# Kernel optimization log

Hardware: AMD Instinct MI355X
Metric: run time of the kernel (lower is better)

The kernel has to match this reference:

```python
import jax, jax.numpy as jnp
import numpy as np

N, E, C_IN, C_OUT, NHEADS = 100000, 1600000, 128, 128, 4


def setup_inputs() -> dict:
    key = jax.random.key(0)
    k1, k2, k3, k4 = jax.random.split(key, 4)
    x = jax.random.normal(k1, (N, C_IN), dtype=jnp.float32)
    edge_index = jax.random.randint(k2, (2, E), 0, N, dtype=jnp.int32)
    batch_slices_x = jnp.array([0, N], dtype=jnp.int32)
    # glorot-style init scale
    weight = jax.random.normal(k3, (C_IN, C_OUT), dtype=jnp.float32) * (1.0 / np.sqrt(C_IN))
    att_weight = jax.random.normal(k4, (1, NHEADS, 2 * (C_OUT // NHEADS)), dtype=jnp.float32) * 0.1
    return {"x": x, "edge_index": edge_index, "batch_slices_x": batch_slices_x,
            "weight": weight, "att_weight": att_weight}


def reference(x, edge_index, batch_slices_x, weight, att_weight):
    # Eval-mode VotePoolLayer: hard attention via per-source-node argmax (scatter_max),
    # cat head-combine, no bias, att_act = identity, then graph pruning (relabel=False).
    n = x.shape[0]
    nheads = att_weight.shape[1]
    c1h = att_weight.shape[2] // 2  # out_channels per head

    h = (x @ weight).reshape(n, nheads, c1h)  # (N, H, c)
    w_j = att_weight[0, :, :c1h]              # (H, c) weights for source (x_j)
    w_i = att_weight[0, :, c1h:]              # (H, c) weights for target (x_i)
    # alpha[e,h] = sum_c h[src[e],h,c]*w_j[h,c] + h[dst[e],h,c]*w_i[h,c]
    s_j = jnp.einsum('nhc,hc->nh', h, w_j)    # (N, H)
    s_i = jnp.einsum('nhc,hc->nh', h, w_i)    # (N, H)

    src, dst = edge_index[0], edge_index[1]
    alpha = s_j[src] + s_i[dst]               # (E, H)

    # scatter_max argmax over edges grouped by src, per head -> one-hot alpha
    e = alpha.shape[0]
    seg_max = jax.ops.segment_max(alpha, src, num_segments=n)  # (N, H)
    is_max = alpha == seg_max[src]                             # (E, H)
    eids = jnp.arange(e, dtype=jnp.int32)[:, None]             # (E, 1)
    cand = jnp.where(is_max, eids, jnp.int32(e))
    seg_argmax = jax.ops.segment_min(cand, src, num_segments=n)  # (N, H) edge ids
    alpha_1hot = (eids == seg_argmax[src]).astype(h.dtype)       # (E, H)

    # message passing: weighted source features, scatter-add at destination
    msg = h[src] * alpha_1hot[:, :, None]                        # (E, H, c)
    out = jax.ops.segment_sum(msg, dst, num_segments=n)          # (N, H, c)
    out = out.reshape(n, nheads * c1h)                           # cat combine

    # edge selection (eval branch): alpha.sum(dim=1) > 0
    edge_select = alpha_1hot.sum(axis=1) > 0                     # (E,)

    # prune (relabel=False): nodes = unique(dst[edge_select]); keep edges with both
    # endpoints in node set; zero out features of the selected nodes.
    node_mask = jnp.zeros(n, dtype=jnp.int32).at[dst].max(edge_select.astype(jnp.int32)) > 0
    edge_keep = node_mask[src] & node_mask[dst]                  # (E,) subgraph edge mask
    x_out = jnp.where(node_mask[:, None], jnp.float32(0), out)

    return x_out, edge_keep, node_mask, batch_slices_x
```

## Files before the change

kernel.cpp:

```cpp
#include <hip/hip_runtime.h>
#include <stdint.h>

typedef unsigned long long u64;
typedef unsigned int u32;
typedef unsigned short u16;
typedef u32 u32x4 __attribute__((ext_vector_type(4)));
typedef float f32x4 __attribute__((ext_vector_type(4)));
typedef int i32x4 __attribute__((ext_vector_type(4)));

#define CIN 128
#define NN 100000
#define EE 1600000

__device__ __forceinline__ float bf2f(u16 v) {
    union { u32 u; float f; } cv;
    cv.u = ((u32)v) << 16;
    return cv.f;
}

__device__ __forceinline__ u16 f2bf(float f) {
    u32 b = __float_as_uint(f);
    return (u16)((b + 0x7FFFu + ((b >> 16) & 1u)) >> 16);
}

__device__ __forceinline__ u16 mono16(u16 b) {
    return (b & 0x8000u) ? (u16)~b : (u16)(b | 0x8000u);
}

__global__ __launch_bounds__(256, 4) void k_s(const u16* __restrict__ x,
                                              const u16* __restrict__ W,
                                              const u16* __restrict__ att,
                                              ushort4* __restrict__ sib,
                                              u32x4* __restrict__ seg16, int n_seg16,
                                              int* __restrict__ nm, int n_nodes) {
    int stride = gridDim.x * blockDim.x;
    int tid = blockIdx.x * blockDim.x + threadIdx.x;
    u32x4 z = { 0, 0, 0, 0 };
    for (int i = tid; i < n_seg16; i += stride) __builtin_nontemporal_store(z, &seg16[i]);
    for (int i = tid; i < n_nodes; i += stride) nm[i] = 0;

    __shared__ float Vl[512];
    for (int slot = threadIdx.x; slot < 512; slot += 256) {
        int k = slot >> 2, head = slot & 3;
        float acc = 0.0f;
        #pragma unroll
        for (int c = 0; c < 32; ++c)
            acc += bf2f(W[k * CIN + head * 32 + c]) * bf2f(att[head * 64 + 32 + c]);
        Vl[slot] = acc;
    }
    __syncthreads();

    for (int n = tid; n < n_nodes; n += stride) {
        const uint4* row = (const uint4*)(x + (size_t)n * CIN);
        float acc[4];
        #pragma unroll
        for (int h = 0; h < 4; ++h) acc[h] = 0.0f;
        #pragma unroll 4
        for (int q = 0; q < 16; ++q) {
            uint4 v = row[q];
            u32 w[4] = { v.x, v.y, v.z, v.w };
            #pragma unroll
            for (int j = 0; j < 4; ++j) {
                float x0 = bf2f((u16)(w[j] & 0xFFFFu));
                float x1 = bf2f((u16)(w[j] >> 16));
                int k0 = q * 8 + j * 2;
                #pragma unroll
                for (int h = 0; h < 4; ++h) acc[h] += x0 * Vl[k0 * 4 + h];
                #pragma unroll
                for (int h = 0; h < 4; ++h) acc[h] += x1 * Vl[(k0 + 1) * 4 + h];
            }
        }
        ushort4 a;
        a.x = mono16(f2bf(acc[0])); a.y = mono16(f2bf(acc[1]));
        a.z = mono16(f2bf(acc[2])); a.w = mono16(f2bf(acc[3]));
        sib[n] = a;
    }
}

__global__ __launch_bounds__(256) void k_edge(const int* __restrict__ ei,
                                              const ushort4* __restrict__ sib,
                                              u64* __restrict__ seg,
                                              u32x4* __restrict__ xout16, int n_xout16,
                                              int n_edges) {
    int t = blockIdx.x * blockDim.x + threadIdx.x;
    int stride = gridDim.x * blockDim.x;
    u32x4 z = { 0, 0, 0, 0 };
    for (int i = t; i < n_xout16; i += stride) __builtin_nontemporal_store(z, &xout16[i]);

    int e = t;
    if (e >= n_edges) return;
    int src = __builtin_nontemporal_load(ei + e);
    int dst = __builtin_nontemporal_load(ei + n_edges + e);
    ushort4 m = sib[dst];
    u64 lo = ((u64)(0x1FFFFFu - (u32)e) << 27) | ((u64)(u32)dst << 10);
    u64* r = seg + (size_t)src * 4;
    ulonglong2 c01 = *(const ulonglong2*)(r);
    ulonglong2 c23 = *(const ulonglong2*)(r + 2);
    u64 k0 = ((u64)m.x << 48) | lo;
    u64 k1 = ((u64)m.y << 48) | lo;
    u64 k2 = ((u64)m.z << 48) | lo;
    u64 k3 = ((u64)m.w << 48) | lo;
    if (k0 > c01.x) atomicMax(&r[0], k0);
    if (k1 > c01.y) atomicMax(&r[1], k1);
    if (k2 > c23.x) atomicMax(&r[2], k2);
    if (k3 > c23.y) atomicMax(&r[3], k3);
}

__global__ void k_select(const u64* __restrict__ seg,
                         int* __restrict__ nm, int n4) {
    int t = blockIdx.x * blockDim.x + threadIdx.x;
    if (t >= n4) return;
    u64 m = seg[t];
    if (m) nm[(int)((m >> 10) & 0x1FFFFu)] = 1;
}

__global__ void k_final(const int* __restrict__ ei, const int* __restrict__ nm,
                        const int* __restrict__ slices, float* __restrict__ out,
                        int n_edges, int n_nodes, int ek_off, int nm_off, int sl_off) {
    int t = blockIdx.x * blockDim.x + threadIdx.x;
    int e0 = 4 * t;
    if (e0 < n_edges) {
        i32x4 srcs = __builtin_nontemporal_load(((const i32x4*)ei) + t);
        i32x4 dsts = __builtin_nontemporal_load(((const i32x4*)(ei + n_edges)) + t);
        f32x4 v;
        v.x = (nm[srcs.x] & nm[dsts.x]) ? 1.0f : 0.0f;
        v.y = (nm[srcs.y] & nm[dsts.y]) ? 1.0f : 0.0f;
        v.z = (nm[srcs.z] & nm[dsts.z]) ? 1.0f : 0.0f;
        v.w = (nm[srcs.w] & nm[dsts.w]) ? 1.0f : 0.0f;
        __builtin_nontemporal_store(v, &((f32x4*)(out + ek_off))[t]);
    }
    if (t < n_nodes) out[nm_off + t] = nm[t] ? 1.0f : 0.0f;
    if (t < 2) out[sl_off + t] = (float)slices[t];
}

extern "C" void kernel_launch(void* const* d_in, const int* in_sizes, int n_in,
                              void* d_out, int out_size, void* d_ws, size_t ws_size,
                              hipStream_t stream) {
    const u16* x = nullptr; const int* ei = nullptr; const int* sl = nullptr;
    const u16* W = nullptr; const u16* att = nullptr;
    for (int i = 0; i < n_in; ++i) {
        switch (in_sizes[i]) {
            case NN * CIN:   x   = (const u16*)d_in[i]; break;
            case 2 * EE:     ei  = (const int*)d_in[i]; break;
            case 2:          sl  = (const int*)d_in[i]; break;
            case CIN * CIN:  W   = (const u16*)d_in[i]; break;
            case 256:        att = (const u16*)d_in[i]; break;
            default: break;
        }
    }
    if (!x || !ei || !sl || !W || !att) return;

    float* out = (float*)d_out;
    const int N = NN;
    const int E = EE;
    const int N4 = N * 4;

    const int ek_off = N * CIN;
    const int nm_off = ek_off + E;
    const int sl_off = nm_off + N;

    char* ws = (char*)d_ws;
    ushort4* sib = (ushort4*)(ws);
    int*     nm  = (int*)    (ws + (size_t)N * 8);
    u64*     seg = (u64*)    (ws + (size_t)N * 12);

    const int n_xout16 = N * CIN / 4;
    const int n_seg16  = N4 / 2;

    k_s<<<1280, 256, 0, stream>>>(x, W, att, sib,
                                  (u32x4*)seg, n_seg16, nm, N);
    k_edge<<<(E + 255) / 256, 256, 0, stream>>>(ei, sib, seg,
                                                (u32x4*)out, n_xout16, E);
    k_select<<<(N4 + 255) / 256, 256, 0, stream>>>(seg, nm, N4);
    k_final<<<(E / 4 + 255) / 256, 256, 0, stream>>>(ei, nm, sl, out, E, N, ek_off, nm_off, sl_off);
}
```

Measured before the change: 197.8 us.

## Fuse select and final passes via cooperative grid sync; two edges per thread

Merges the node-select kernel and the final edge-mask kernel into one cooperative kernel. A grid-wide sync separates the phase that marks selected nodes from the phase that writes the edge, node-mask and slice outputs, which removes one kernel launch and its gap. The edge kernel now handles two edges per thread with vectorized index loads, for more memory-level parallelism per thread. The cooperative launch relies on all 1563 blocks being co-resident, and the grid sync adds its own barrier cost.

Result: slower. 389.2 us (+96.7%).

```diff
diff --git a/kernel.cpp b/kernel.cpp
--- a/kernel.cpp
+++ b/kernel.cpp
@@ -1,5 +1,8 @@
 #include <hip/hip_runtime.h>
+#include <hip/hip_cooperative_groups.h>
 #include <stdint.h>
+
+namespace cg = cooperative_groups;
 
 typedef unsigned long long u64;
 typedef unsigned int u32;
@@ -7,6 +10,7 @@
 typedef u32 u32x4 __attribute__((ext_vector_type(4)));
 typedef float f32x4 __attribute__((ext_vector_type(4)));
 typedef int i32x4 __attribute__((ext_vector_type(4)));
+typedef int i32x2 __attribute__((ext_vector_type(2)));
 
 #define CIN 128
 #define NN 100000
@@ -87,39 +91,57 @@
     u32x4 z = { 0, 0, 0, 0 };
     for (int i = t; i < n_xout16; i += stride) __builtin_nontemporal_store(z, &xout16[i]);
 
-    int e = t;
-    if (e >= n_edges) return;
-    int src = __builtin_nontemporal_load(ei + e);
-    int dst = __builtin_nontemporal_load(ei + n_edges + e);
-    ushort4 m = sib[dst];
-    u64 lo = ((u64)(0x1FFFFFu - (u32)e) << 27) | ((u64)(u32)dst << 10);
-    u64* r = seg + (size_t)src * 4;
-    ulonglong2 c01 = *(const ulonglong2*)(r);
-    ulonglong2 c23 = *(const ulonglong2*)(r + 2);
-    u64 k0 = ((u64)m.x << 48) | lo;
-    u64 k1 = ((u64)m.y << 48) | lo;
-    u64 k2 = ((u64)m.z << 48) | lo;
-    u64 k3 = ((u64)m.w << 48) | lo;
-    if (k0 > c01.x) atomicMax(&r[0], k0);
-    if (k1 > c01.y) atomicMax(&r[1], k1);
-    if (k2 > c23.x) atomicMax(&r[2], k2);
-    if (k3 > c23.y) atomicMax(&r[3], k3);
-}
-
-__global__ void k_select(const u64* __restrict__ seg,
-                         int* __restrict__ nm, int n4) {
+    int e0 = 2 * t;
+    if (e0 >= n_edges) return;
+    i32x2 s2 = __builtin_nontemporal_load(((const i32x2*)ei) + t);
+    i32x2 d2 = __builtin_nontemporal_load(((const i32x2*)(ei + n_edges)) + t);
+    ushort4 m0 = sib[d2.x];
+    ushort4 m1 = sib[d2.y];
+    u64* r0 = seg + (size_t)s2.x * 4;
+    u64* r1 = seg + (size_t)s2.y * 4;
+
+    {
+        ulonglong2 c01 = *(const ulonglong2*)(r0);
+        ulonglong2 c23 = *(const ulonglong2*)(r0 + 2);
+        u64 lo = ((u64)(0x1FFFFFu - (u32)e0) << 27) | ((u64)(u32)d2.x << 10);
+        u64 k0 = ((u64)m0.x << 48) | lo;
+        u64 k1 = ((u64)m0.y << 48) | lo;
+        u64 k2 = ((u64)m0.z << 48) | lo;
+        u64 k3 = ((u64)m0.w << 48) | lo;
+        if (k0 > c01.x) atomicMax(&r0[0], k0);
+        if (k1 > c01.y) atomicMax(&r0[1], k1);
+        if (k2 > c23.x) atomicMax(&r0[2], k2);
+        if (k3 > c23.y) atomicMax(&r0[3], k3);
+    }
+    {
+        ulonglong2 c01 = *(const ulonglong2*)(r1);
+        ulonglong2 c23 = *(const ulonglong2*)(r1 + 2);
+        u64 lo = ((u64)(0x1FFFFFu - (u32)(e0 + 1)) << 27) | ((u64)(u32)d2.y << 10);
+        u64 k0 = ((u64)m1.x << 48) | lo;
+        u64 k1 = ((u64)m1.y << 48) | lo;
+        u64 k2 = ((u64)m1.z << 48) | lo;
+        u64 k3 = ((u64)m1.w << 48) | lo;
+        if (k0 > c01.x) atomicMax(&r1[0], k0);
+        if (k1 > c01.y) atomicMax(&r1[1], k1);
+        if (k2 > c23.x) atomicMax(&r1[2], k2);
+        if (k3 > c23.y) atomicMax(&r1[3], k3);
+    }
+}
+
+__global__ __launch_bounds__(256) void k_sf(const int* __restrict__ ei,
+                                            const u64* __restrict__ seg,
+                                            int* nm,
+                                            const int* __restrict__ slices,
+                                            float* __restrict__ out,
+                                            int n4, int n_edges, int n_nodes,
+                                            int ek_off, int nm_off, int sl_off) {
     int t = blockIdx.x * blockDim.x + threadIdx.x;
-    if (t >= n4) return;
-    u64 m = seg[t];
-    if (m) nm[(int)((m >> 10) & 0x1FFFFu)] = 1;
-}
-
-__global__ void k_final(const int* __restrict__ ei, const int* __restrict__ nm,
-                        const int* __restrict__ slices, float* __restrict__ out,
-                        int n_edges, int n_nodes, int ek_off, int nm_off, int sl_off) {
-    int t = blockIdx.x * blockDim.x + threadIdx.x;
-    int e0 = 4 * t;
-    if (e0 < n_edges) {
+    if (t < n4) {
+        u64 m = seg[t];
+        if (m) nm[(int)((m >> 10) & 0x1FFFFu)] = 1;
+    }
+    cg::this_grid().sync();
+    if (4 * t < n_edges) {
         i32x4 srcs = __builtin_nontemporal_load(((const i32x4*)ei) + t);
         i32x4 dsts = __builtin_nontemporal_load(((const i32x4*)(ei + n_edges)) + t);
         f32x4 v;
@@ -153,11 +175,11 @@
     float* out = (float*)d_out;
     const int N = NN;
     const int E = EE;
-    const int N4 = N * 4;
-
-    const int ek_off = N * CIN;
-    const int nm_off = ek_off + E;
-    const int sl_off = nm_off + N;
+    int N4 = N * 4;
+
+    int ek_off = N * CIN;
+    int nm_off = ek_off + E;
+    int sl_off = nm_off + N;
 
     char* ws = (char*)d_ws;
     ushort4* sib = (ushort4*)(ws);
@@ -169,8 +191,13 @@
 
     k_s<<<1280, 256, 0, stream>>>(x, W, att, sib,
                                   (u32x4*)seg, n_seg16, nm, N);
-    k_edge<<<(E + 255) / 256, 256, 0, stream>>>(ei, sib, seg,
-                                                (u32x4*)out, n_xout16, E);
-    k_select<<<(N4 + 255) / 256, 256, 0, stream>>>(seg, nm, N4);
-    k_final<<<(E / 4 + 255) / 256, 256, 0, stream>>>(ei, nm, sl, out, E, N, ek_off, nm_off, sl_off);
-}
+    k_edge<<<(E / 2 + 255) / 256, 256, 0, stream>>>(ei, sib, seg,
+                                                    (u32x4*)out, n_xout16, E);
+
+    int n_edges = E, n_nodes = N;
+    void* args[] = { (void*)&ei, (void*)&seg, (void*)&nm, (void*)&sl, (void*)&out,
+                     (void*)&N4, (void*)&n_edges, (void*)&n_nodes,
+                     (void*)&ek_off, (void*)&nm_off, (void*)&sl_off };
+    hipLaunchCooperativeKernel((const void*)k_sf, dim3((N4 + 255) / 256), dim3(256),
+                               args, 0, stream);
+}
```
